# Performance work log

Measured on AMD Instinct MI355X. Metric: run time of the kernel, lower is better.

The kernel has to match this reference:

```python
import jax, jax.numpy as jnp
import numpy as np

B, C, H, W_IMG = 16, 3, 384, 384
P = 16
G = H // P                 # 24
NPATCH = G * G             # 576
SEQ = NPATCH + 1           # 577 (with cls token)
D, FF, NH, NL = 768, 3072, 12, 12
NCLS = 1000
K = int(0.5 * NPATCH)
HD = D // NH
EPS = 1e-6


def _ln(x, g, b):
    mu = jnp.mean(x, axis=-1, keepdims=True)
    var = jnp.mean((x - mu) ** 2, axis=-1, keepdims=True)
    return (x - mu) * jax.lax.rsqrt(var + EPS) * g + b


def setup_inputs() -> dict:
    key = jax.random.key(0)
    ks = jax.random.split(key, 12)
    s = 0.02
    return {
        "x": jax.random.normal(ks[0], (B, C, H, W_IMG), jnp.float32),
        "patch_w": jax.random.normal(ks[1], (D, C, P, P), jnp.float32) * s,
        "patch_b": jnp.zeros((D,), jnp.float32),
        "cls_tok": jax.random.normal(ks[2], (1, 1, D), jnp.float32) * s,
        "pos_emb": jax.random.normal(ks[3], (1, SEQ, D), jnp.float32) * s,
        "ln1_g": jnp.ones((NL, D), jnp.float32),
        "ln1_b": jnp.zeros((NL, D), jnp.float32),
        "Wqkv": jax.random.normal(ks[4], (NL, D, 3 * D), jnp.float32) * s,
        "bqkv": jnp.zeros((NL, 3 * D), jnp.float32),
        "Wo": jax.random.normal(ks[5], (NL, D, D), jnp.float32) * s,
        "bo": jnp.zeros((NL, D), jnp.float32),
        "ln2_g": jnp.ones((NL, D), jnp.float32),
        "ln2_b": jnp.zeros((NL, D), jnp.float32),
        "W1": jax.random.normal(ks[6], (NL, D, FF), jnp.float32) * s,
        "b1": jnp.zeros((NL, FF), jnp.float32),
        "W2": jax.random.normal(ks[7], (NL, FF, D), jnp.float32) * s,
        "b2": jnp.zeros((NL, D), jnp.float32),
        "lnf_g": jnp.ones((D,), jnp.float32),
        "lnf_b": jnp.zeros((D,), jnp.float32),
        "fc_w": jax.random.normal(ks[8], (D, NCLS), jnp.float32) * s,
        "fc_b": jnp.zeros((NCLS,), jnp.float32),
    }


def reference(x, patch_w, patch_b, cls_tok, pos_emb, ln1_g, ln1_b, Wqkv, bqkv,
              Wo, bo, ln2_g, ln2_b, W1, b1, W2, b2, lnf_g, lnf_b, fc_w, fc_b):
    b = x.shape[0]
    # patch embedding: strided conv -> (b, D, G, G) -> (b, NPATCH, D)
    patches = jax.lax.conv_general_dilated(
        x, patch_w, window_strides=(P, P), padding="VALID",
        dimension_numbers=("NCHW", "OIHW", "NCHW")) + patch_b[None, :, None, None]
    tok = patches.reshape(b, D, NPATCH).transpose(0, 2, 1)
    tok = jnp.concatenate([jnp.broadcast_to(cls_tok, (b, 1, D)), tok], axis=1)
    tok = tok + pos_emb  # seq matches original_seq_len, no resize

    # saliency = avg-pool of raw first input channel (net_G output is unused in the source)
    pooled = x[:, 0].reshape(b, G, P, G, P).mean(axis=(2, 4)).reshape(b, NPATCH)
    _, idx = jax.lax.top_k(jnp.abs(pooled), K)          # (b, K)
    spatial = tok[:, 1:, :]
    sel = jnp.take_along_axis(spatial, idx[:, :, None], axis=1)  # (b, K, D)
    h = jnp.concatenate([tok[:, :1, :], sel], axis=1)   # (b, K+1, D)
    S = h.shape[1]

    scale = 1.0 / np.sqrt(HD)
    for i in range(NL):
        y = _ln(h, ln1_g[i], ln1_b[i])
        qkv = y @ Wqkv[i] + bqkv[i]
        q, k_, v = jnp.split(qkv, 3, axis=-1)
        q = q.reshape(b, S, NH, HD)
        k_ = k_.reshape(b, S, NH, HD)
        v = v.reshape(b, S, NH, HD)
        att = jnp.einsum("bqhd,bkhd->bhqk", q, k_) * scale
        att = jax.nn.softmax(att, axis=-1)
        o = jnp.einsum("bhqk,bkhd->bqhd", att, v).reshape(b, S, D)
        h = h + (o @ Wo[i] + bo[i])
        y = _ln(h, ln2_g[i], ln2_b[i])
        h = h + (jax.nn.gelu(y @ W1[i] + b1[i], approximate=False) @ W2[i] + b2[i])

    cls_out = _ln(h, lnf_g, lnf_b)[:, 0]   # pool_type='tok'
    return cls_out @ fc_w + fc_b


if __name__ == "__main__":
    out = reference(**setup_inputs())
    print(out.shape)
```

## Files before the change

### kernel.cpp

```cpp
#include <hip/hip_runtime.h>
#include <hip/hip_bf16.h>
#include <math.h>

#define BB 16
#define SS 289
#define DD 768
#define FFD 3072
#define NHD 12
#define NLAY 12
#define KSEL 288
#define NPATCH 576

typedef short bf16x8 __attribute__((ext_vector_type(8)));
typedef short bf16x4 __attribute__((ext_vector_type(4)));
typedef float f32x4 __attribute__((ext_vector_type(4)));

typedef __attribute__((address_space(3))) void lds_t;
typedef __attribute__((address_space(1))) const void glb_t;

__device__ __forceinline__ void gload16(const void* g, void* l) {
    __builtin_amdgcn_global_load_lds((glb_t*)g, (lds_t*)l, 16, 0, 0);
}

__device__ __forceinline__ bf16x8 ds_read128(unsigned addr) {
    bf16x8 r;
    asm volatile("ds_read_b128 %0, %1" : "=v"(r) : "v"(addr));
    return r;
}

__device__ __forceinline__ float gelu_f(float v) {
    return 0.5f * v * (1.0f + erff(v * 0.70710678118654752f));
}

__device__ __forceinline__ void store_val(float* p, float v) { *p = v; }
__device__ __forceinline__ void store_val(__hip_bfloat16* p, float v) { *p = __float2bfloat16(v); }

__global__ __launch_bounds__(256) void pool_kernel(const float* __restrict__ x,
                                                   float* __restrict__ pooled) {
    int bp = blockIdx.x;
    int b = bp / NPATCH, p = bp - b * NPATCH;
    int gi = p / 24, gj = p - gi * 24;
    int tid = threadIdx.x;
    int pi = tid >> 4, pj = tid & 15;
    float v = x[((size_t)(b * 3) * 384 + gi * 16 + pi) * 384 + gj * 16 + pj];
    #pragma unroll
    for (int o = 32; o > 0; o >>= 1) v += __shfl_down(v, o);
    __shared__ float red[4];
    if ((tid & 63) == 0) red[tid >> 6] = v;
    __syncthreads();
    if (tid == 0) pooled[bp] = (red[0] + red[1] + red[2] + red[3]) * (1.0f / 256.0f);
}

__global__ __launch_bounds__(576) void topk_kernel(const float* __restrict__ pooled,
                                                   int* __restrict__ idxsel) {
    __shared__ float a[NPATCH];
    int b = blockIdx.x, tid = threadIdx.x;
    a[tid] = fabsf(pooled[b * NPATCH + tid]);
    __syncthreads();
    float mine = a[tid];
    int rank = 0;
    for (int j = 0; j < NPATCH; ++j) {
        float aj = a[j];
        rank += (aj > mine) || (aj == mine && j < tid);
    }
    if (rank < KSEL) idxsel[b * KSEL + rank] = tid;
}

__global__ __launch_bounds__(256) void convert_bf16(const float* __restrict__ in,
                                                    __hip_bfloat16* __restrict__ out,
                                                    int n) {
    int i = blockIdx.x * 256 + threadIdx.x;
    if (i < n) out[i] = __float2bfloat16(in[i]);
}

__global__ __launch_bounds__(256) void convert_layer(const float* __restrict__ wqkv,
                                                     const float* __restrict__ wo,
                                                     const float* __restrict__ w1,
                                                     const float* __restrict__ w2,
                                                     __hip_bfloat16* __restrict__ oqkv,
                                                     __hip_bfloat16* __restrict__ owo,
                                                     __hip_bfloat16* __restrict__ ow1,
                                                     __hip_bfloat16* __restrict__ ow2) {
    __shared__ float tb[32][33];
    int bid = blockIdx.x;
    const float* W; __hip_bfloat16* O; int K, N, tile;
    if (bid < 1728)      { W = wqkv; O = oqkv; K = 768;  N = 2304; tile = bid; }
    else if (bid < 2304) { W = wo;   O = owo;  K = 768;  N = 768;  tile = bid - 1728; }
    else if (bid < 4608) { W = w1;   O = ow1;  K = 768;  N = 3072; tile = bid - 2304; }
    else                 { W = w2;   O = ow2;  K = 3072; N = 768;  tile = bid - 4608; }
    int ntx = N >> 5;
    int n0 = (tile % ntx) << 5, k0 = (tile / ntx) << 5;
    int t = threadIdx.x;
    int r = t >> 3, c = (t & 7) << 2;
    float4 v = *(const float4*)&W[(size_t)(k0 + r) * N + n0 + c];
    tb[r][c] = v.x; tb[r][c + 1] = v.y; tb[r][c + 2] = v.z; tb[r][c + 3] = v.w;
    __syncthreads();
    int n = t >> 3, k = (t & 7) << 2;
    __hip_bfloat16* dst = &O[(size_t)(n0 + n) * K + k0 + k];
    #pragma unroll
    for (int j = 0; j < 4; ++j) dst[j] = __float2bfloat16(tb[k + j][n]);
}

__global__ __launch_bounds__(256) void im2col_kernel(const float* __restrict__ x,
                                                     const int* __restrict__ idxsel,
                                                     __hip_bfloat16* __restrict__ col) {
    int t = blockIdx.x;
    int b = t / KSEL, r = t - b * KSEL;
    int p = idxsel[b * KSEL + r];
    int gi = p / 24, gj = p - gi * 24;
    int tid = threadIdx.x;
    int pi = tid >> 4, pj = tid & 15;
    __hip_bfloat16* crow = col + (size_t)t * 768;
    #pragma unroll
    for (int c = 0; c < 3; ++c)
        crow[c * 256 + tid] = __float2bfloat16(
            x[((size_t)(b * 3 + c) * 384 + gi * 16 + pi) * 384 + gj * 16 + pj]);
}

__global__ __launch_bounds__(256) void assemble_tokens(const float* __restrict__ temp,
                                                       const float* __restrict__ cls_tok,
                                                       const float* __restrict__ pos_emb,
                                                       const int* __restrict__ idxsel,
                                                       float* __restrict__ h) {
    int row = blockIdx.x;
    int b = row / SS, s = row - b * SS;
    int tid = threadIdx.x;
    float* hrow = h + (size_t)row * DD;
    if (s == 0) {
        #pragma unroll
        for (int c = 0; c < 3; ++c) {
            int j = c * 256 + tid;
            hrow[j] = cls_tok[j] + pos_emb[j];
        }
    } else {
        int r = s - 1;
        int p = idxsel[b * KSEL + r];
        const float* trow = temp + (size_t)(b * KSEL + r) * DD;
        const float* pe = pos_emb + (size_t)(1 + p) * DD;
        #pragma unroll
        for (int c = 0; c < 3; ++c) {
            int j = c * 256 + tid;
            hrow[j] = trow[j] + pe[j];
        }
    }
}

template <typename T>
__global__ __launch_bounds__(256) void ln_kernel(const float* __restrict__ in,
                                                 T* __restrict__ out,
                                                 const float* __restrict__ g,
                                                 const float* __restrict__ be,
                                                 size_t in_stride) {
    int row = blockIdx.x;
    const float* r = in + (size_t)row * in_stride;
    T* w = out + (size_t)row * DD;
    int tid = threadIdx.x;
    float v0 = r[tid], v1 = r[256 + tid], v2 = r[512 + tid];
    float s = v0 + v1 + v2;
    #pragma unroll
    for (int o = 32; o > 0; o >>= 1) s += __shfl_down(s, o);
    __shared__ float red[4];
    if ((tid & 63) == 0) red[tid >> 6] = s;
    __syncthreads();
    float mu = (red[0] + red[1] + red[2] + red[3]) * (1.0f / 768.0f);
    float d0 = v0 - mu, d1 = v1 - mu, d2 = v2 - mu;
    float q = d0 * d0 + d1 * d1 + d2 * d2;
    #pragma unroll
    for (int o = 32; o > 0; o >>= 1) q += __shfl_down(q, o);
    __syncthreads();
    if ((tid & 63) == 0) red[tid >> 6] = q;
    __syncthreads();
    float var = (red[0] + red[1] + red[2] + red[3]) * (1.0f / 768.0f);
    float rs = rsqrtf(var + 1e-6f);
    store_val(&w[tid],       d0 * rs * g[tid]       + be[tid]);
    store_val(&w[256 + tid], d1 * rs * g[256 + tid] + be[256 + tid]);
    store_val(&w[512 + tid], d2 * rs * g[512 + tid] + be[512 + tid]);
}

template <typename OUT_T, int ACT, int RES>
__global__ __launch_bounds__(256) void gemm_bf16(const __hip_bfloat16* __restrict__ A,
                                                 const __hip_bfloat16* __restrict__ BT,
                                                 OUT_T* __restrict__ C,
                                                 const float* __restrict__ bias,
                                                 const float* __restrict__ res,
                                                 int M, int N, int K) {
    __shared__ __hip_bfloat16 smA[3][128 * 32];
    __shared__ __hip_bfloat16 smB[3][128 * 32];
    const int t = threadIdx.x;
    const int lane = t & 63, wid = t >> 6;
    const int wr = wid >> 1, wc = wid & 1;
    const int l15 = lane & 15, l4 = lane >> 4;

    const int gx = gridDim.x;
    const int nwg = gx * gridDim.y;
    const int orig = blockIdx.y * gx + blockIdx.x;
    const int q8 = nwg >> 3, r8 = nwg & 7;
    const int xcd = orig & 7, linb = orig >> 3;
    const int swz = (xcd < r8 ? xcd * (q8 + 1) : r8 * (q8 + 1) + (xcd - r8) * q8) + linb;
    const int m0 = (swz / gx) << 7;
    const int n0 = (swz - (swz / gx) * gx) << 7;

    int ra[4], rb[4];
    #pragma unroll
    for (int f = 0; f < 4; ++f) {
        int ml = wr * 64 + f * 16 + l15;
        ra[f] = ml * 64 + ((l4 ^ ((ml >> 1) & 3)) << 4);
        int nl = wc * 64 + f * 16 + l15;
        rb[f] = nl * 64 + ((l4 ^ ((nl >> 1) & 3)) << 4);
    }

    size_t aoff[2], boff[2];
    #pragma unroll
    for (int it = 0; it < 2; ++it) {
        int s = it * 256 + t;
        int m = s >> 2;
        int kc = (s & 3) ^ ((m >> 1) & 3);
        int gm = m0 + m; if (gm > M - 1) gm = M - 1;
        aoff[it] = (size_t)gm * K + kc * 8;
        boff[it] = (size_t)(n0 + m) * K + kc * 8;
    }
    const int wb = wid << 10;
    const unsigned ldsA0 = (unsigned)(size_t)(lds_t*)&smA[0][0];
    const unsigned ldsB0 = (unsigned)(size_t)(lds_t*)&smB[0][0];

    auto STAGE = [&](int kt, int buf) {
        int k0e = kt << 5;
        gload16(A + aoff[0] + k0e, (char*)(&smA[buf][0]) + wb);
        gload16(A + aoff[1] + k0e, (char*)(&smA[buf][0]) + wb + 4096);
        gload16(BT + boff[0] + k0e, (char*)(&smB[buf][0]) + wb);
        gload16(BT + boff[1] + k0e, (char*)(&smB[buf][0]) + wb + 4096);
    };

    f32x4 acc[4][4];
    #pragma unroll
    for (int i = 0; i < 4; ++i)
        #pragma unroll
        for (int j = 0; j < 4; ++j) acc[i][j] = (f32x4){0.f, 0.f, 0.f, 0.f};

    const int nt = K >> 5;
    STAGE(0, 0); STAGE(1, 1);
    int cur = 0, stb = 2;
    for (int kt = 0; kt < nt; ++kt) {
        if (kt + 1 < nt) asm volatile("s_waitcnt vmcnt(4)" ::: "memory");
        else             asm volatile("s_waitcnt vmcnt(0)" ::: "memory");
        asm volatile("s_barrier" ::: "memory");
        if (kt + 2 < nt) STAGE(kt + 2, stb);
        const unsigned sa = ldsA0 + cur * 8192u;
        const unsigned sb = ldsB0 + cur * 8192u;
        bf16x8 af[4], bf[4];
        #pragma unroll
        for (int f = 0; f < 4; ++f) {
            af[f] = ds_read128(sa + ra[f]);
            bf[f] = ds_read128(sb + rb[f]);
        }
        asm volatile("s_waitcnt lgkmcnt(0)" ::: "memory");
        __builtin_amdgcn_sched_barrier(0);
        #pragma unroll
        for (int i = 0; i < 4; ++i)
            #pragma unroll
            for (int j = 0; j < 4; ++j)
                acc[i][j] = __builtin_amdgcn_mfma_f32_16x16x32_bf16(af[i], bf[j], acc[i][j], 0, 0, 0);
        cur = cur == 2 ? 0 : cur + 1;
        stb = stb == 2 ? 0 : stb + 1;
    }

    #pragma unroll
    for (int i = 0; i < 4; ++i) {
        int gmb = m0 + wr * 64 + i * 16 + l4 * 4;
        #pragma unroll
        for (int j = 0; j < 4; ++j) {
            int gn = n0 + wc * 64 + j * 16 + l15;
            float bv = bias ? bias[gn] : 0.f;
            #pragma unroll
            for (int r = 0; r < 4; ++r) {
                int gm = gmb + r;
                if (gm < M) {
                    float v = acc[i][j][r] + bv;
                    if (ACT) v = gelu_f(v);
                    if (RES) v += res[(size_t)gm * N + gn];
                    store_val(&C[(size_t)gm * N + gn], v);
                }
            }
        }
    }
}

__global__ __launch_bounds__(64) void attn_fused(const __hip_bfloat16* __restrict__ qkv,
                                                 __hip_bfloat16* __restrict__ o) {
    __shared__ __hip_bfloat16 p_lds[32][40];
    __shared__ __hip_bfloat16 v_lds[32][68];
    const int qt = blockIdx.x, bh = blockIdx.y;
    const int b = bh / NHD, hd = bh - b * NHD;
    const int lane = threadIdx.x;
    const int l15 = lane & 15, l4 = lane >> 4;
    const size_t tb = (size_t)b * SS;
    const int hc = hd * 64;

    bf16x8 aq[2][2];
    #pragma unroll
    for (int qi = 0; qi < 2; ++qi) {
        int qr = qt * 32 + qi * 16 + l15;
        if (qr >= SS) qr = SS - 1;
        const __hip_bfloat16* qrow = qkv + (tb + qr) * 2304 + hc;
        #pragma unroll
        for (int kd = 0; kd < 2; ++kd)
            aq[qi][kd] = *(const bf16x8*)(qrow + kd * 32 + l4 * 8);
    }

    float m_run[2][4], l_run[2][4];
    f32x4 oa[2][4];
    #pragma unroll
    for (int qi = 0; qi < 2; ++qi)
        #pragma unroll
        for (int r = 0; r < 4; ++r) { m_run[qi][r] = -1e30f; l_run[qi][r] = 0.f; }
    #pragma unroll
    for (int qi = 0; qi < 2; ++qi)
        #pragma unroll
        for (int dt = 0; dt < 4; ++dt) oa[qi][dt] = (f32x4){0.f, 0.f, 0.f, 0.f};

    for (int kt = 0; kt < 10; ++kt) {
        const int kbase = kt * 32;
        bf16x4 vreg[8];
        #pragma unroll
        for (int it = 0; it < 8; ++it) {
            int vr = kbase + it * 4 + l4;
            if (vr >= SS) vr = SS - 1;
            vreg[it] = *(const bf16x4*)(qkv + (tb + vr) * 2304 + 1536 + hc + l15 * 4);
        }
        bf16x8 bk[2][2];
        #pragma unroll
        for (int ki = 0; ki < 2; ++ki) {
            int kr = kbase + ki * 16 + l15;
            if (kr >= SS) kr = SS - 1;
            const __hip_bfloat16* krow = qkv + (tb + kr) * 2304 + 768 + hc;
            #pragma unroll
            for (int kd = 0; kd < 2; ++kd)
                bk[ki][kd] = *(const bf16x8*)(krow + kd * 32 + l4 * 8);
        }
        f32x4 s[2][2];
        #pragma unroll
        for (int qi = 0; qi < 2; ++qi)
            #pragma unroll
            for (int ki = 0; ki < 2; ++ki) {
                f32x4 a = (f32x4){0.f, 0.f, 0.f, 0.f};
                #pragma unroll
                for (int kd = 0; kd < 2; ++kd)
                    a = __builtin_amdgcn_mfma_f32_16x16x32_bf16(aq[qi][kd], bk[ki][kd], a, 0, 0, 0);
                s[qi][ki] = a;
            }
        #pragma unroll
        for (int ki = 0; ki < 2; ++ki) {
            bool valid = (kbase + ki * 16 + l15) < SS;
            #pragma unroll
            for (int qi = 0; qi < 2; ++qi)
                #pragma unroll
                for (int r = 0; r < 4; ++r)
                    s[qi][ki][r] = valid ? s[qi][ki][r] * 0.125f : -1e30f;
        }
        float p[2][2][4];
        #pragma unroll
        for (int qi = 0; qi < 2; ++qi) {
            float tm[4];
            #pragma unroll
            for (int r = 0; r < 4; ++r) tm[r] = fmaxf(s[qi][0][r], s[qi][1][r]);
            #pragma unroll
            for (int sh = 1; sh < 16; sh <<= 1)
                #pragma unroll
                for (int r = 0; r < 4; ++r) tm[r] = fmaxf(tm[r], __shfl_xor(tm[r], sh));
            float rs[4];
            #pragma unroll
            for (int r = 0; r < 4; ++r) {
                float mn = fmaxf(m_run[qi][r], tm[r]);
                float corr = __expf(m_run[qi][r] - mn);
                m_run[qi][r] = mn;
                float p0 = __expf(s[qi][0][r] - mn);
                float p1 = __expf(s[qi][1][r] - mn);
                p[qi][0][r] = p0; p[qi][1][r] = p1;
                rs[r] = p0 + p1;
                l_run[qi][r] *= corr;
                #pragma unroll
                for (int dt = 0; dt < 4; ++dt) oa[qi][dt][r] *= corr;
            }
            #pragma unroll
            for (int sh = 1; sh < 16; sh <<= 1)
                #pragma unroll
                for (int r = 0; r < 4; ++r) rs[r] += __shfl_xor(rs[r], sh);
            #pragma unroll
            for (int r = 0; r < 4; ++r) l_run[qi][r] += rs[r];
        }
        #pragma unroll
        for (int qi = 0; qi < 2; ++qi)
            #pragma unroll
            for (int ki = 0; ki < 2; ++ki)
                #pragma unroll
                for (int r = 0; r < 4; ++r)
                    p_lds[qi * 16 + l4 * 4 + r][ki * 16 + l15] = __float2bfloat16(p[qi][ki][r]);
        #pragma unroll
        for (int it = 0; it < 8; ++it)
            *(bf16x4*)&v_lds[it * 4 + l4][l15 * 4] = vreg[it];
        __syncthreads();
        bf16x8 pa[2];
        #pragma unroll
        for (int qi = 0; qi < 2; ++qi)
            pa[qi] = *(const bf16x8*)&p_lds[qi * 16 + l15][l4 * 8];
        bf16x8 vb[4];
        #pragma unroll
        for (int dt = 0; dt < 4; ++dt) {
            bf16x8 v;
            #pragma unroll
            for (int j = 0; j < 8; ++j)
                v[j] = *(const short*)&v_lds[l4 * 8 + j][dt * 16 + l15];
            vb[dt] = v;
        }
        #pragma unroll
        for (int qi = 0; qi < 2; ++qi)
            #pragma unroll
            for (int dt = 0; dt < 4; ++dt)
                oa[qi][dt] = __builtin_amdgcn_mfma_f32_16x16x32_bf16(pa[qi], vb[dt], oa[qi][dt], 0, 0, 0);
        __syncthreads();
    }
    #pragma unroll
    for (int qi = 0; qi < 2; ++qi)
        #pragma unroll
        for (int r = 0; r < 4; ++r) {
            int q = qt * 32 + qi * 16 + l4 * 4 + r;
            if (q < SS) {
                float inv = 1.0f / l_run[qi][r];
                __hip_bfloat16* orow = o + (tb + q) * 768 + hc;
                #pragma unroll
                for (int dt = 0; dt < 4; ++dt)
                    orow[dt * 16 + l15] = __float2bfloat16(oa[qi][dt][r] * inv);
            }
        }
}

__global__ __launch_bounds__(256) void gemm_f32(const float* __restrict__ A,
                                                const float* __restrict__ Bm,
                                                float* __restrict__ Cm,
                                                const float* __restrict__ bias,
                                                int M, int N, int Kd) {
    __shared__ float As[16][68];
    __shared__ float Bs[16][64];
    int tid = threadIdx.x;
    int m0 = blockIdx.y << 6;
    int n0 = blockIdx.x << 6;
    int tx = tid & 15, ty = tid >> 4;
    int arow = tid >> 2, acol = (tid & 3) << 2;
    int brow = tid >> 4, bcol = (tid & 15) << 2;
    float acc[4][4] = {};
    for (int k0 = 0; k0 < Kd; k0 += 16) {
        float4 av = make_float4(0.f, 0.f, 0.f, 0.f);
        int gm = m0 + arow;
        if (gm < M) av = *(const float4*)&A[(size_t)gm * Kd + k0 + acol];
        As[acol + 0][arow] = av.x;
        As[acol + 1][arow] = av.y;
        As[acol + 2][arow] = av.z;
        As[acol + 3][arow] = av.w;
        float4 bv = make_float4(0.f, 0.f, 0.f, 0.f);
        int gn = n0 + bcol;
        const float* brp = &Bm[(size_t)(k0 + brow) * N];
        if (gn + 3 < N) bv = *(const float4*)&brp[gn];
        else if (gn < N) {
            bv.x = brp[gn];
            if (gn + 1 < N) bv.y = brp[gn + 1];
            if (gn + 2 < N) bv.z = brp[gn + 2];
        }
        *(float4*)&Bs[brow][bcol] = bv;
        __syncthreads();
        #pragma unroll
        for (int kk = 0; kk < 16; ++kk) {
            float a[4], b[4];
            *(float4*)a = *(const float4*)&As[kk][ty << 2];
            *(float4*)b = *(const float4*)&Bs[kk][tx << 2];
            #pragma unroll
            for (int i = 0; i < 4; ++i)
                #pragma unroll
                for (int j = 0; j < 4; ++j)
                    acc[i][j] = fmaf(a[i], b[j], acc[i][j]);
        }
        __syncthreads();
    }
    #pragma unroll
    for (int i = 0; i < 4; ++i) {
        int gm = m0 + (ty << 2) + i;
        if (gm >= M) continue;
        #pragma unroll
        for (int j = 0; j < 4; ++j) {
            int gn = n0 + (tx << 2) + j;
            if (gn >= N) continue;
            Cm[(size_t)gm * N + gn] = acc[i][j] + (bias ? bias[gn] : 0.f);
        }
    }
}

static const size_t OFF_POOLED = 0;
static const size_t OFF_IDX    = 10240;
static const size_t OFF_H      = 16384;
static const size_t OFF_YB     = 3567616;
static const size_t OFF_OB     = 5343232;
static const size_t OFF_QKVB   = 7118848;
static const size_t OFF_WBUF   = 12445696;
static const size_t OFF_PWB    = 15984640;
static const size_t OFF_YF     = 16279552;
static const size_t OFF_BIG    = 16291840;

extern "C" void kernel_launch(void* const* d_in, const int* in_sizes, int n_in,
                              void* d_out, int out_size, void* d_ws, size_t ws_size,
                              hipStream_t stream) {
    const float* x       = (const float*)d_in[0];
    const float* patch_w = (const float*)d_in[1];
    const float* patch_b = (const float*)d_in[2];
    const float* cls_tok = (const float*)d_in[3];
    const float* pos_emb = (const float*)d_in[4];
    const float* ln1_g   = (const float*)d_in[5];
    const float* ln1_b   = (const float*)d_in[6];
    const float* Wqkv    = (const float*)d_in[7];
    const float* bqkv    = (const float*)d_in[8];
    const float* Wo      = (const float*)d_in[9];
    const float* bo      = (const float*)d_in[10];
    const float* ln2_g   = (const float*)d_in[11];
    const float* ln2_b   = (const float*)d_in[12];
    const float* W1      = (const float*)d_in[13];
    const float* b1      = (const float*)d_in[14];
    const float* W2      = (const float*)d_in[15];
    const float* b2      = (const float*)d_in[16];
    const float* lnf_g   = (const float*)d_in[17];
    const float* lnf_b   = (const float*)d_in[18];
    const float* fc_w    = (const float*)d_in[19];
    const float* fc_b    = (const float*)d_in[20];
    float* out = (float*)d_out;
    float* ws  = (float*)d_ws;

    float*          pooled = ws + OFF_POOLED;
    int*            idxsel = (int*)(ws + OFF_IDX);
    float*          h      = ws + OFF_H;
    __hip_bfloat16* yb     = (__hip_bfloat16*)(ws + OFF_YB);
    __hip_bfloat16* ob     = (__hip_bfloat16*)(ws + OFF_OB);
    __hip_bfloat16* qkvb   = (__hip_bfloat16*)(ws + OFF_QKVB);
    __hip_bfloat16* wbuf   = (__hip_bfloat16*)(ws + OFF_WBUF);
    __hip_bfloat16* pwb    = (__hip_bfloat16*)(ws + OFF_PWB);
    float*          yf     = ws + OFF_YF;
    float*          big    = ws + OFF_BIG;
    __hip_bfloat16* col    = (__hip_bfloat16*)big;
    float*          temp   = big + 1769472;
    __hip_bfloat16* hidden = (__hip_bfloat16*)big;

    __hip_bfloat16* wqkvT = wbuf;
    __hip_bfloat16* woT   = wbuf + 1769472;
    __hip_bfloat16* w1T   = wbuf + 2359296;
    __hip_bfloat16* w2T   = wbuf + 4718592;

    pool_kernel<<<BB * NPATCH, 256, 0, stream>>>(x, pooled);
    topk_kernel<<<BB, 576, 0, stream>>>(pooled, idxsel);
    convert_bf16<<<(589824 + 255) / 256, 256, 0, stream>>>(patch_w, pwb, 589824);
    im2col_kernel<<<BB * KSEL, 256, 0, stream>>>(x, idxsel, col);
    gemm_bf16<float, 0, 0><<<dim3(6, 36), 256, 0, stream>>>(col, pwb, temp, patch_b,
                                                            nullptr, 4608, DD, DD);
    assemble_tokens<<<BB * SS, 256, 0, stream>>>(temp, cls_tok, pos_emb, idxsel, h);

    const int M = BB * SS;
    const int MG = 37;

    for (int i = 0; i < NLAY; ++i) {
        convert_layer<<<6912, 256, 0, stream>>>(Wqkv + (size_t)i * DD * 3 * DD,
                                                Wo + (size_t)i * DD * DD,
                                                W1 + (size_t)i * DD * FFD,
                                                W2 + (size_t)i * FFD * DD,
                                                wqkvT, woT, w1T, w2T);

        ln_kernel<__hip_bfloat16><<<M, 256, 0, stream>>>(h, yb, ln1_g + i * DD, ln1_b + i * DD, DD);
        gemm_bf16<__hip_bfloat16, 0, 0><<<dim3(18, MG), 256, 0, stream>>>(
            yb, wqkvT, qkvb, bqkv + (size_t)i * 3 * DD, nullptr, M, 3 * DD, DD);
        attn_fused<<<dim3(10, BB * NHD), 64, 0, stream>>>(qkvb, ob);
        gemm_bf16<float, 0, 1><<<dim3(6, MG), 256, 0, stream>>>(
            ob, woT, h, bo + (size_t)i * DD, h, M, DD, DD);
        ln_kernel<__hip_bfloat16><<<M, 256, 0, stream>>>(h, yb, ln2_g + i * DD, ln2_b + i * DD, DD);
        gemm_bf16<__hip_bfloat16, 1, 0><<<dim3(24, MG), 256, 0, stream>>>(
            yb, w1T, hidden, b1 + (size_t)i * FFD, nullptr, M, FFD, DD);
        gemm_bf16<float, 0, 1><<<dim3(6, MG), 256, 0, stream>>>(
            hidden, w2T, h, b2 + (size_t)i * DD, h, M, DD, FFD);
    }

    ln_kernel<float><<<BB, 256, 0, stream>>>(h, yf, lnf_g, lnf_b, (size_t)SS * DD);
    gemm_f32<<<dim3(16, 1), 256, 0, stream>>>(yf, fc_w, out, fc_b, BB, 1000, DD);
}
```

Baseline: 2.918 ms.

## Widen GEMM tiles to 128x256 with 8 waves and split-K for N=768 GEMMs

The bf16 GEMM now uses 512 threads (8 waves) and a 128x256 output tile, which halves the grid along N and reuses each A tile across twice as many columns. The Wo and W2 projections, which have N=768 and few tiles, use split-K (2 and 4 ways). Their fp32 partials go to a workspace buffer and a separate combine kernel sums them with the bias and residual. The classifier head's fp32 GEMM is replaced by a simple LDS-cached kernel. The cost is extra partial-sum traffic and an extra launch per split GEMM, plus more LDS per block.

```diff
diff --git a/kernel.cpp b/kernel.cpp
--- a/kernel.cpp
+++ b/kernel.cpp
@@ -177,18 +177,19 @@
     store_val(&w[512 + tid], d2 * rs * g[512 + tid] + be[512 + tid]);
 }
 
-template <typename OUT_T, int ACT, int RES>
-__global__ __launch_bounds__(256) void gemm_bf16(const __hip_bfloat16* __restrict__ A,
+template <typename OUT_T, int ACT, int RES, int SPLITK>
+__global__ __launch_bounds__(512) void gemm_bf16(const __hip_bfloat16* __restrict__ A,
                                                  const __hip_bfloat16* __restrict__ BT,
                                                  OUT_T* __restrict__ C,
                                                  const float* __restrict__ bias,
                                                  const float* __restrict__ res,
+                                                 float* __restrict__ part,
                                                  int M, int N, int K) {
     __shared__ __hip_bfloat16 smA[3][128 * 32];
-    __shared__ __hip_bfloat16 smB[3][128 * 32];
+    __shared__ __hip_bfloat16 smB[3][256 * 32];
     const int t = threadIdx.x;
     const int lane = t & 63, wid = t >> 6;
-    const int wr = wid >> 1, wc = wid & 1;
+    const int wr = wid >> 2, wc = wid & 3;
     const int l15 = lane & 15, l4 = lane >> 4;
 
     const int gx = gridDim.x;
@@ -198,7 +199,10 @@
     const int xcd = orig & 7, linb = orig >> 3;
     const int swz = (xcd < r8 ? xcd * (q8 + 1) : r8 * (q8 + 1) + (xcd - r8) * q8) + linb;
     const int m0 = (swz / gx) << 7;
-    const int n0 = (swz - (swz / gx) * gx) << 7;
+    const int n0 = (swz - (swz / gx) * gx) << 8;
+
+    const int Ksub = K / SPLITK;
+    const int kz0 = blockIdx.z * Ksub;
 
     int ra[4], rb[4];
     #pragma unroll
@@ -209,15 +213,19 @@
         rb[f] = nl * 64 + ((l4 ^ ((nl >> 1) & 3)) << 4);
     }
 
-    size_t aoff[2], boff[2];
-    #pragma unroll
-    for (int it = 0; it < 2; ++it) {
-        int s = it * 256 + t;
-        int m = s >> 2;
-        int kc = (s & 3) ^ ((m >> 1) & 3);
-        int gm = m0 + m; if (gm > M - 1) gm = M - 1;
-        aoff[it] = (size_t)gm * K + kc * 8;
-        boff[it] = (size_t)(n0 + m) * K + kc * 8;
+    size_t aoff, boff[2];
+    {
+        int mA = t >> 2;
+        int kcA = (t & 3) ^ ((mA >> 1) & 3);
+        int gmA = m0 + mA; if (gmA > M - 1) gmA = M - 1;
+        aoff = (size_t)gmA * K + kz0 + kcA * 8;
+        #pragma unroll
+        for (int it = 0; it < 2; ++it) {
+            int s = it * 512 + t;
+            int mB = s >> 2;
+            int kc = (s & 3) ^ ((mB >> 1) & 3);
+            boff[it] = (size_t)(n0 + mB) * K + kz0 + kc * 8;
+        }
     }
     const int wb = wid << 10;
     const unsigned ldsA0 = (unsigned)(size_t)(lds_t*)&smA[0][0];
@@ -225,10 +233,9 @@
 
     auto STAGE = [&](int kt, int buf) {
         int k0e = kt << 5;
-        gload16(A + aoff[0] + k0e, (char*)(&smA[buf][0]) + wb);
-        gload16(A + aoff[1] + k0e, (char*)(&smA[buf][0]) + wb + 4096);
+        gload16(A + aoff + k0e,     (char*)(&smA[buf][0]) + wb);
         gload16(BT + boff[0] + k0e, (char*)(&smB[buf][0]) + wb);
-        gload16(BT + boff[1] + k0e, (char*)(&smB[buf][0]) + wb + 4096);
+        gload16(BT + boff[1] + k0e, (char*)(&smB[buf][0]) + 8192 + wb);
     };
 
     f32x4 acc[4][4];
@@ -237,16 +244,16 @@
         #pragma unroll
         for (int j = 0; j < 4; ++j) acc[i][j] = (f32x4){0.f, 0.f, 0.f, 0.f};
 
-    const int nt = K >> 5;
+    const int nt = Ksub >> 5;
     STAGE(0, 0); STAGE(1, 1);
     int cur = 0, stb = 2;
     for (int kt = 0; kt < nt; ++kt) {
-        if (kt + 1 < nt) asm volatile("s_waitcnt vmcnt(4)" ::: "memory");
+        if (kt + 1 < nt) asm volatile("s_waitcnt vmcnt(3)" ::: "memory");
         else             asm volatile("s_waitcnt vmcnt(0)" ::: "memory");
         asm volatile("s_barrier" ::: "memory");
         if (kt + 2 < nt) STAGE(kt + 2, stb);
         const unsigned sa = ldsA0 + cur * 8192u;
-        const unsigned sb = ldsB0 + cur * 8192u;
+        const unsigned sb = ldsB0 + cur * 16384u;
         bf16x8 af[4], bf[4];
         #pragma unroll
         for (int f = 0; f < 4; ++f) {
@@ -264,25 +271,88 @@
         stb = stb == 2 ? 0 : stb + 1;
     }
 
-    #pragma unroll
-    for (int i = 0; i < 4; ++i) {
-        int gmb = m0 + wr * 64 + i * 16 + l4 * 4;
-        #pragma unroll
-        for (int j = 0; j < 4; ++j) {
-            int gn = n0 + wc * 64 + j * 16 + l15;
-            float bv = bias ? bias[gn] : 0.f;
-            #pragma unroll
-            for (int r = 0; r < 4; ++r) {
-                int gm = gmb + r;
-                if (gm < M) {
-                    float v = acc[i][j][r] + bv;
-                    if (ACT) v = gelu_f(v);
-                    if (RES) v += res[(size_t)gm * N + gn];
-                    store_val(&C[(size_t)gm * N + gn], v);
+    if (SPLITK == 1) {
+        #pragma unroll
+        for (int i = 0; i < 4; ++i) {
+            int gmb = m0 + wr * 64 + i * 16 + l4 * 4;
+            #pragma unroll
+            for (int j = 0; j < 4; ++j) {
+                int gn = n0 + wc * 64 + j * 16 + l15;
+                float bv = bias ? bias[gn] : 0.f;
+                #pragma unroll
+                for (int r = 0; r < 4; ++r) {
+                    int gm = gmb + r;
+                    if (gm < M) {
+                        float v = acc[i][j][r] + bv;
+                        if (ACT) v = gelu_f(v);
+                        if (RES) v += res[(size_t)gm * N + gn];
+                        store_val(&C[(size_t)gm * N + gn], v);
+                    }
                 }
             }
         }
-    }
+    } else {
+        float* pz = part + (size_t)blockIdx.z * M * N;
+        #pragma unroll
+        for (int i = 0; i < 4; ++i) {
+            int gmb = m0 + wr * 64 + i * 16 + l4 * 4;
+            #pragma unroll
+            for (int j = 0; j < 4; ++j) {
+                int gn = n0 + wc * 64 + j * 16 + l15;
+                #pragma unroll
+                for (int r = 0; r < 4; ++r) {
+                    int gm = gmb + r;
+                    if (gm < M) pz[(size_t)gm * N + gn] = acc[i][j][r];
+                }
+            }
+        }
+    }
+}
+
+template <int NPART>
+__global__ __launch_bounds__(256) void combine_res(const float* __restrict__ part,
+                                                   const float* __restrict__ bias,
+                                                   float* __restrict__ h,
+                                                   int MN, int N) {
+    int i = (blockIdx.x * 256 + threadIdx.x) * 4;
+    if (i >= MN) return;
+    float4 v = *(const float4*)&part[i];
+    #pragma unroll
+    for (int z = 1; z < NPART; ++z) {
+        float4 p = *(const float4*)&part[(size_t)z * MN + i];
+        v.x += p.x; v.y += p.y; v.z += p.z; v.w += p.w;
+    }
+    int n = i % N;
+    float4 bv = *(const float4*)&bias[n];
+    float4 hv = *(const float4*)&h[i];
+    v.x += bv.x + hv.x; v.y += bv.y + hv.y; v.z += bv.z + hv.z; v.w += bv.w + hv.w;
+    *(float4*)&h[i] = v;
+}
+
+__global__ __launch_bounds__(256) void head_gemm(const float* __restrict__ yf,
+                                                 const float* __restrict__ fc_w,
+                                                 const float* __restrict__ fc_b,
+                                                 float* __restrict__ out) {
+    __shared__ float ylds[4 * 768];
+    const int tid = threadIdx.x;
+    const int mh = blockIdx.y * 4;
+    for (int i = tid; i < 4 * 768; i += 256) ylds[i] = yf[(size_t)(mh + (i >> 9) * 0 + i / 768) * 768 + i % 768];
+    __syncthreads();
+    const int n = blockIdx.x * 256 + tid;
+    if (n >= 1000) return;
+    float acc0 = 0.f, acc1 = 0.f, acc2 = 0.f, acc3 = 0.f;
+    for (int k = 0; k < 768; ++k) {
+        float w = fc_w[(size_t)k * 1000 + n];
+        acc0 = fmaf(ylds[k], w, acc0);
+        acc1 = fmaf(ylds[768 + k], w, acc1);
+        acc2 = fmaf(ylds[1536 + k], w, acc2);
+        acc3 = fmaf(ylds[2304 + k], w, acc3);
+    }
+    float b = fc_b[n];
+    out[(size_t)(mh + 0) * 1000 + n] = acc0 + b;
+    out[(size_t)(mh + 1) * 1000 + n] = acc1 + b;
+    out[(size_t)(mh + 2) * 1000 + n] = acc2 + b;
+    out[(size_t)(mh + 3) * 1000 + n] = acc3 + b;
 }
 
 __global__ __launch_bounds__(64) void attn_fused(const __hip_bfloat16* __restrict__ qkv,
@@ -434,65 +504,6 @@
         }
 }
 
-__global__ __launch_bounds__(256) void gemm_f32(const float* __restrict__ A,
-                                                const float* __restrict__ Bm,
-                                                float* __restrict__ Cm,
-                                                const float* __restrict__ bias,
-                                                int M, int N, int Kd) {
-    __shared__ float As[16][68];
-    __shared__ float Bs[16][64];
-    int tid = threadIdx.x;
-    int m0 = blockIdx.y << 6;
-    int n0 = blockIdx.x << 6;
-    int tx = tid & 15, ty = tid >> 4;
-    int arow = tid >> 2, acol = (tid & 3) << 2;
-    int brow = tid >> 4, bcol = (tid & 15) << 2;
-    float acc[4][4] = {};
-    for (int k0 = 0; k0 < Kd; k0 += 16) {
-        float4 av = make_float4(0.f, 0.f, 0.f, 0.f);
-        int gm = m0 + arow;
-        if (gm < M) av = *(const float4*)&A[(size_t)gm * Kd + k0 + acol];
-        As[acol + 0][arow] = av.x;
-        As[acol + 1][arow] = av.y;
-        As[acol + 2][arow] = av.z;
-        As[acol + 3][arow] = av.w;
-        float4 bv = make_float4(0.f, 0.f, 0.f, 0.f);
-        int gn = n0 + bcol;
-        const float* brp = &Bm[(size_t)(k0 + brow) * N];
-        if (gn + 3 < N) bv = *(const float4*)&brp[gn];
-        else if (gn < N) {
-            bv.x = brp[gn];
-            if (gn + 1 < N) bv.y = brp[gn + 1];
-            if (gn + 2 < N) bv.z = brp[gn + 2];
-        }
-        *(float4*)&Bs[brow][bcol] = bv;
-        __syncthreads();
-        #pragma unroll
-        for (int kk = 0; kk < 16; ++kk) {
-            float a[4], b[4];
-            *(float4*)a = *(const float4*)&As[kk][ty << 2];
-            *(float4*)b = *(const float4*)&Bs[kk][tx << 2];
-            #pragma unroll
-            for (int i = 0; i < 4; ++i)
-                #pragma unroll
-                for (int j = 0; j < 4; ++j)
-                    acc[i][j] = fmaf(a[i], b[j], acc[i][j]);
-        }
-        __syncthreads();
-    }
-    #pragma unroll
-    for (int i = 0; i < 4; ++i) {
-        int gm = m0 + (ty << 2) + i;
-        if (gm >= M) continue;
-        #pragma unroll
-        for (int j = 0; j < 4; ++j) {
-            int gn = n0 + (tx << 2) + j;
-            if (gn >= N) continue;
-            Cm[(size_t)gm * N + gn] = acc[i][j] + (bias ? bias[gn] : 0.f);
-        }
-    }
-}
-
 static const size_t OFF_POOLED = 0;
 static const size_t OFF_IDX    = 10240;
 static const size_t OFF_H      = 16384;
@@ -503,6 +514,7 @@
 static const size_t OFF_PWB    = 15984640;
 static const size_t OFF_YF     = 16279552;
 static const size_t OFF_BIG    = 16291840;
+static const size_t OFF_PART   = 23394304;
 
 extern "C" void kernel_launch(void* const* d_in, const int* in_sizes, int n_in,
                               void* d_out, int out_size, void* d_ws, size_t ws_size,
@@ -541,6 +553,7 @@
     __hip_bfloat16* pwb    = (__hip_bfloat16*)(ws + OFF_PWB);
     float*          yf     = ws + OFF_YF;
     float*          big    = ws + OFF_BIG;
+    float*          part   = ws + OFF_PART;
     __hip_bfloat16* col    = (__hip_bfloat16*)big;
     float*          temp   = big + 1769472;
     __hip_bfloat16* hidden = (__hip_bfloat16*)big;
@@ -550,16 +563,17 @@
     __hip_bfloat16* w1T   = wbuf + 2359296;
     __hip_bfloat16* w2T   = wbuf + 4718592;
 
+    const int M = BB * SS;
+    const int MG = 37;
+    const int MN = M * DD;
+
     pool_kernel<<<BB * NPATCH, 256, 0, stream>>>(x, pooled);
     topk_kernel<<<BB, 576, 0, stream>>>(pooled, idxsel);
     convert_bf16<<<(589824 + 255) / 256, 256, 0, stream>>>(patch_w, pwb, 589824);
     im2col_kernel<<<BB * KSEL, 256, 0, stream>>>(x, idxsel, col);
-    gemm_bf16<float, 0, 0><<<dim3(6, 36), 256, 0, stream>>>(col, pwb, temp, patch_b,
-                                                            nullptr, 4608, DD, DD);
+    gemm_bf16<float, 0, 0, 1><<<dim3(3, 36), 512, 0, stream>>>(
+        col, pwb, temp, patch_b, nullptr, nullptr, 4608, DD, DD);
     assemble_tokens<<<BB * SS, 256, 0, stream>>>(temp, cls_tok, pos_emb, idxsel, h);
-
-    const int M = BB * SS;
-    const int MG = 37;
 
     for (int i = 0; i < NLAY; ++i) {
         convert_layer<<<6912, 256, 0, stream>>>(Wqkv + (size_t)i * DD * 3 * DD,
@@ -569,18 +583,20 @@
                                                 wqkvT, woT, w1T, w2T);
 
         ln_kernel<__hip_bfloat16><<<M, 256, 0, stream>>>(h, yb, ln1_g + i * DD, ln1_b + i * DD, DD);
-        gemm_bf16<__hip_bfloat16, 0, 0><<<dim3(18, MG), 256, 0, stream>>>(
-            yb, wqkvT, qkvb, bqkv + (size_t)i * 3 * DD, nullptr, M, 3 * DD, DD);
+        gemm_bf16<__hip_bfloat16, 0, 0, 1><<<dim3(9, MG), 512, 0, stream>>>(
+            yb, wqkvT, qkvb, bqkv + (size_t)i * 3 * DD, nullptr, nullptr, M, 3 * DD, DD);
         attn_fused<<<dim3(10, BB * NHD), 64, 0, stream>>>(qkvb, ob);
-        gemm_bf16<float, 0, 1><<<dim3(6, MG), 256, 0, stream>>>(
-            ob, woT, h, bo + (size_t)i * DD, h, M, DD, DD);
+        gemm_bf16<float, 0, 0, 2><<<dim3(3, MG, 2), 512, 0, stream>>>(
+            ob, woT, (float*)nullptr, nullptr, nullptr, part, M, DD, DD);
+        combine_res<2><<<(MN / 4 + 255) / 256, 256, 0, stream>>>(part, bo + (size_t)i * DD, h, MN, DD);
         ln_kernel<__hip_bfloat16><<<M, 256, 0, stream>>>(h, yb, ln2_g + i * DD, ln2_b + i * DD, DD);
-        gemm_bf16<__hip_bfloat16, 1, 0><<<dim3(24, MG), 256, 0, stream>>>(
-            yb, w1T, hidden, b1 + (size_t)i * FFD, nullptr, M, FFD, DD);
-        gemm_bf16<float, 0, 1><<<dim3(6, MG), 256, 0, stream>>>(
-            hidden, w2T, h, b2 + (size_t)i * DD, h, M, DD, FFD);
+        gemm_bf16<__hip_bfloat16, 1, 0, 1><<<dim3(12, MG), 512, 0, stream>>>(
+            yb, w1T, hidden, b1 + (size_t)i * FFD, nullptr, nullptr, M, FFD, DD);
+        gemm_bf16<float, 0, 0, 4><<<dim3(3, MG, 4), 512, 0, stream>>>(
+            hidden, w2T, (float*)nullptr, nullptr, nullptr, part, M, DD, FFD);
+        combine_res<4><<<(MN / 4 + 255) / 256, 256, 0, stream>>>(part, b2 + (size_t)i * DD, h, MN, DD);
     }
 
     ln_kernel<float><<<BB, 256, 0, stream>>>(h, yf, lnf_g, lnf_b, (size_t)SS * DD);
-    gemm_f32<<<dim3(16, 1), 256, 0, stream>>>(yf, fc_w, out, fc_b, BB, 1000, DD);
-}
+    head_gemm<<<dim3(4, 4), 256, 0, stream>>>(yf, fc_w, fc_b, out);
+}
```

Measured after the change: 2.464 ms. 1.18x faster.
